# Kernel optimization log

Measured on AMD Instinct MI355X. Metric: run time of the kernel, lower is better.

## Reference

```python
import jax, jax.numpy as jnp
import numpy as np

NUM_HEADS = 4
D_MODEL = 256
HEAD_DIM = D_MODEL // NUM_HEADS  # 64
B, N = 8, 2048


def _proj(x, W, b):
    # Conv1d with kernel_size=1 == pointwise linear over channel dim
    # x: [B, C_in, N], W: [C_out, C_in], b: [C_out]
    return jnp.einsum('oi,bin->bon', W, x) + b[None, :, None]


def setup_inputs() -> dict:
    key = jax.random.key(0)
    ks = jax.random.split(key, 11)
    s = 1.0 / np.sqrt(D_MODEL)
    return {
        'query': jax.random.normal(ks[0], (B, D_MODEL, N), jnp.float32),
        'key':   jax.random.normal(ks[1], (B, D_MODEL, N), jnp.float32),
        'value': jax.random.normal(ks[2], (B, D_MODEL, N), jnp.float32),
        'Wq': jax.random.normal(ks[3], (D_MODEL, D_MODEL), jnp.float32) * s,
        'bq': jax.random.normal(ks[4], (D_MODEL,), jnp.float32) * 0.01,
        'Wk': jax.random.normal(ks[5], (D_MODEL, D_MODEL), jnp.float32) * s,
        'bk': jax.random.normal(ks[6], (D_MODEL,), jnp.float32) * 0.01,
        'Wv': jax.random.normal(ks[7], (D_MODEL, D_MODEL), jnp.float32) * s,
        'bv': jax.random.normal(ks[8], (D_MODEL,), jnp.float32) * 0.01,
        'Wm': jax.random.normal(ks[9], (D_MODEL, D_MODEL), jnp.float32) * s,
        'bm': jax.random.normal(ks[10], (D_MODEL,), jnp.float32) * 0.01,
    }


def reference(query, key, value, Wq, bq, Wk, bk, Wv, bv, Wm, bm):
    b = query.shape[0]
    # project then split channels into (head_dim, num_heads): [B, d, h, N]
    q = _proj(query, Wq, bq).reshape(b, HEAD_DIM, NUM_HEADS, -1)
    k = _proj(key,   Wk, bk).reshape(b, HEAD_DIM, NUM_HEADS, -1)
    v = _proj(value, Wv, bv).reshape(b, HEAD_DIM, NUM_HEADS, -1)
    scale = 1.0 / jnp.sqrt(jnp.asarray(HEAD_DIM, q.dtype))
    scores = jnp.einsum('bdhn,bdhm->bhnm', q, k) * scale  # [B,H,N,N]
    prob = jax.nn.softmax(scores, axis=-1)
    x = jnp.einsum('bhnm,bdhm->bdhn', prob, v)  # [B,d,H,N]
    x = x.reshape(b, HEAD_DIM * NUM_HEADS, -1)  # [B, d_model, N]
    return _proj(x, Wm, bm)
```

## Files before the change

### kernel.cpp

```cpp
#include <hip/hip_runtime.h>
#include <math.h>


constexpr int BATCH  = 8;
constexpr int DMODEL = 256;
constexpr int SEQ    = 2048;
constexpr int HDIM   = 64;
constexpr int TN     = 128;
constexpr int TM     = 64;
constexpr int NJT    = SEQ / TM;

typedef _Float16 half4_t __attribute__((ext_vector_type(4)));
typedef _Float16 half8_t __attribute__((ext_vector_type(8)));
typedef float    float4_t __attribute__((ext_vector_type(4)));

static __device__ __forceinline__ void ld16_lds(const void* g, void* l) {
    __builtin_amdgcn_global_load_lds(
        (const __attribute__((address_space(1))) unsigned*)g,
        (__attribute__((address_space(3))) unsigned*)l, 16, 0, 0);
}

__global__ __launch_bounds__(256)
void prep_w(const float* __restrict__ Wq, const float* __restrict__ Wk,
            const float* __restrict__ Wv, const float* __restrict__ Wm,
            _Float16* __restrict__ wf)
{
    const int which = blockIdx.y;
    const float* src = which == 0 ? Wq : which == 1 ? Wk : which == 2 ? Wv : Wm;
    const int i = (blockIdx.x * 256 + threadIdx.x) * 4;
    const float4 v = *(const float4*)&src[i];
    half4_t o; o[0] = v.x; o[1] = v.y; o[2] = v.z; o[3] = v.w;
    *(half4_t*)&wf[(size_t)which * DMODEL * DMODEL + i] = o;
}

__global__ __launch_bounds__(256, 3)
void gemm_qkv(const _Float16* __restrict__ wf, const float* __restrict__ bq,
              const float* __restrict__ bk, const float* __restrict__ bv,
              const float* __restrict__ Xq, const float* __restrict__ Xk,
              const float* __restrict__ Xv, _Float16* __restrict__ qT,
              _Float16* __restrict__ kT, _Float16* __restrict__ vT)
{
    const int n0 = blockIdx.x * 64;
    const int proj = blockIdx.y >> 3, b = blockIdx.y & 7;
    const _Float16* W    = wf + (size_t)proj * DMODEL * DMODEL;
    const float*    bias = proj == 0 ? bq : proj == 1 ? bk : bv;
    const float*    X    = (proj == 0 ? Xq : proj == 1 ? Xk : Xv)
                           + (size_t)b * DMODEL * SEQ;

    __shared__ __align__(16) char lds[50432];
    float*    T  = (float*)lds;
    _Float16* Xs = (_Float16*)(lds + 16640);
    _Float16* Tw = (_Float16*)lds;

    const int tid = threadIdx.x, tn = tid & 15, tc = tid >> 4;

    #pragma unroll
    for (int cc = 0; cc < 4; ++cc) {
        __syncthreads();
        #pragma unroll
        for (int i = 0; i < 4; ++i) {
            const int c = tc + 16 * i;
            const float4 v = *(const float4*)&X[(size_t)(cc * 64 + c) * SEQ + n0 + tn * 4];
            T[c * 65 + tn * 4 + 0] = v.x; T[c * 65 + tn * 4 + 1] = v.y;
            T[c * 65 + tn * 4 + 2] = v.z; T[c * 65 + tn * 4 + 3] = v.w;
        }
        __syncthreads();
        #pragma unroll
        for (int i = 0; i < 4; ++i) {
            const int n = tc + 16 * i;
            half4_t h4;
            #pragma unroll
            for (int j = 0; j < 4; ++j) h4[j] = (_Float16)T[(tn * 4 + j) * 65 + n];
            *(half4_t*)&Xs[n * 264 + cc * 64 + tn * 4] = h4;
        }
    }
    __syncthreads();

    const int w = tid >> 6, lane = tid & 63;
    const int lm = lane & 15, g = lane >> 4, g8 = g * 8;
    const int cw0 = w * 64;

    float4_t acc[4][4];
    #pragma unroll
    for (int mt = 0; mt < 4; ++mt)
        #pragma unroll
        for (int nt = 0; nt < 4; ++nt) acc[mt][nt] = (float4_t){0.f, 0.f, 0.f, 0.f};

    #pragma unroll
    for (int k0 = 0; k0 < DMODEL; k0 += 64) {
        half8_t a[4][2], bb[4][2];
        #pragma unroll
        for (int mt = 0; mt < 4; ++mt)
            #pragma unroll
            for (int kd = 0; kd < 2; ++kd)
                a[mt][kd] = *(const half8_t*)&W[(size_t)(cw0 + mt * 16 + lm) * DMODEL
                                                + k0 + kd * 32 + g8];
        #pragma unroll
        for (int nt = 0; nt < 4; ++nt)
            #pragma unroll
            for (int kd = 0; kd < 2; ++kd)
                bb[nt][kd] = *(const half8_t*)&Xs[(nt * 16 + lm) * 264
                                                  + k0 + kd * 32 + g8];
        #pragma unroll
        for (int kd = 0; kd < 2; ++kd)
            #pragma unroll
            for (int mt = 0; mt < 4; ++mt)
                #pragma unroll
                for (int nt = 0; nt < 4; ++nt)
                    acc[mt][nt] = __builtin_amdgcn_mfma_f32_16x16x32_f16(
                        a[mt][kd], bb[nt][kd], acc[mt][nt], 0, 0, 0);
    }
    __syncthreads();

    #pragma unroll
    for (int mt = 0; mt < 4; ++mt) {
        const float4 b4 = *(const float4*)&bias[cw0 + mt * 16 + g * 4];
        const float bb4[4] = {b4.x, b4.y, b4.z, b4.w};
        #pragma unroll
        for (int nt = 0; nt < 4; ++nt) {
            half4_t pk;
            #pragma unroll
            for (int r = 0; r < 4; ++r) pk[r] = (_Float16)(acc[mt][nt][r] + bb4[r]);
            *(half4_t*)&Tw[((w * 64 + nt * 16 + lm)) * 68 + mt * 16 + g * 4] = pk;
        }
    }

    if (proj < 2) {
        _Float16* dst = (proj == 0 ? qT : kT);
        const int h2 = lane >> 4, lml = lane & 15;
        #pragma unroll
        for (int it = 0; it < 4; ++it) {
            const int nl = it * 16 + lml;
            #pragma unroll
            for (int dc = 0; dc < 2; ++dc) {
                half8_t ch;
                #pragma unroll
                for (int e = 0; e < 8; ++e)
                    ch[e] = Tw[(w * 64 + nl) * 68 + 4 * (dc * 8 + e) + h2];
                const int chunk = (w * 2 + dc) ^ (nl & 7);
                *(half8_t*)&dst[((size_t)(b * 4 + h2) * SEQ + n0 + nl) * HDIM
                                + chunk * 8] = ch;
            }
        }
    } else {
        const int hh = lane & 3, dl = (lane >> 2) & 15;
        const int d = w * 16 + dl;
        const size_t rowbase =
            (((size_t)(b * 4 + hh) * NJT + (n0 >> 6)) * HDIM + d) * (size_t)TM;
        #pragma unroll
        for (int jc = 0; jc < 8; ++jc) {
            half8_t ch;
            #pragma unroll
            for (int e = 0; e < 8; ++e)
                ch[e] = Tw[(w * 64 + jc * 8 + e) * 68 + 4 * dl + hh];
            *(half8_t*)&vT[rowbase + ((jc ^ (dl & 7)) << 3)] = ch;
        }
    }
}

__global__ __launch_bounds__(256, 4)
void attn_f16(const _Float16* __restrict__ qT, const _Float16* __restrict__ kT,
              const _Float16* __restrict__ vT, _Float16* __restrict__ xa,
              _Float16* __restrict__ xb, float* __restrict__ rs)
{
    const int bh = blockIdx.z, b = bh >> 2, h = bh & 3;
    const int jh = blockIdx.y;
    const int tid = threadIdx.x, wid = tid >> 6, lane = tid & 63;
    const int lm = lane & 15, g = lane >> 4;
    const int i0 = blockIdx.x * TN + wid * 32;

    __shared__ _Float16 Kb[2][TM * HDIM];
    __shared__ _Float16 Vb[2][TM * HDIM];

    half8_t bq[2][2];
    const _Float16* qbase = qT + (size_t)bh * SEQ * HDIM;
    #pragma unroll
    for (int rt = 0; rt < 2; ++rt)
        #pragma unroll
        for (int kd = 0; kd < 2; ++kd) {
            const int row = i0 + rt * 16 + lm;
            half8_t r8 = *(const half8_t*)(qbase + (size_t)row * HDIM
                                           + (((kd * 4 + g) ^ (lm & 7)) << 3));
            #pragma unroll
            for (int e = 0; e < 8; ++e) r8[e] = r8[e] * (_Float16)0.125f;
            bq[rt][kd] = r8;
        }

    const char* kt = (const char*)(kT + ((size_t)bh * SEQ + jh * (SEQ / 2)) * HDIM);
    const char* vt = (const char*)(vT + ((size_t)bh * NJT + jh * 16) * TM * HDIM);

    float4_t o[2][4], o5[2];
    #pragma unroll
    for (int rt = 0; rt < 2; ++rt) {
        #pragma unroll
        for (int dt = 0; dt < 4; ++dt) o[rt][dt] = (float4_t){0.f, 0.f, 0.f, 0.f};
        o5[rt] = (float4_t){0.f, 0.f, 0.f, 0.f};
    }
    const half4_t vone = {(_Float16)1.f, (_Float16)1.f, (_Float16)1.f, (_Float16)1.f};

    #define STAGE(jt, bu)                                                     \
        {                                                                     \
            const char* kg = kt + (size_t)(jt) * 8192;                        \
            const char* vg = vt + (size_t)(jt) * 8192;                        \
            _Pragma("unroll")                                                 \
            for (int p = 0; p < 2; ++p) {                                     \
                const int c = wid + p * 4;                                    \
                ld16_lds(kg + c * 1024 + lane * 16, (char*)&Kb[bu][0] + c * 1024); \
                ld16_lds(vg + c * 1024 + lane * 16, (char*)&Vb[bu][0] + c * 1024); \
            }                                                                 \
        }

    STAGE(0, 0);
    __syncthreads();

    for (int jt = 0; jt < 16; ++jt) {
        const int cur = jt & 1;
        if (jt + 1 < 16) STAGE(jt + 1, cur ^ 1);

        float4_t s[4][2];
        #pragma unroll
        for (int ct = 0; ct < 4; ++ct)
            #pragma unroll
            for (int rt = 0; rt < 2; ++rt) s[ct][rt] = (float4_t){0.f, 0.f, 0.f, 0.f};
        #pragma unroll
        for (int kd = 0; kd < 2; ++kd)
            #pragma unroll
            for (int ct = 0; ct < 4; ++ct) {
                const half8_t fk = *(const half8_t*)
                    &Kb[cur][(ct * 16 + lm) * HDIM + (((kd * 4 + g) ^ (lm & 7)) << 3)];
                #pragma unroll
                for (int rt = 0; rt < 2; ++rt)
                    s[ct][rt] = __builtin_amdgcn_mfma_f32_16x16x32_f16(
                        fk, bq[rt][kd], s[ct][rt], 0, 0, 0);
            }

        half4_t ap[4][2];
        #pragma unroll
        for (int ct = 0; ct < 4; ++ct)
            #pragma unroll
            for (int rt = 0; rt < 2; ++rt)
                #pragma unroll
                for (int r = 0; r < 4; ++r)
                    ap[ct][rt][r] = (_Float16)__expf(s[ct][rt][r]);
        #pragma unroll
        for (int ct = 0; ct < 4; ++ct)
            #pragma unroll
            for (int rt = 0; rt < 2; ++rt)
                o5[rt] = __builtin_amdgcn_mfma_f32_16x16x16f16(
                    ap[ct][rt], vone, o5[rt], 0, 0, 0);

        #pragma unroll
        for (int ct = 0; ct < 4; ++ct)
            #pragma unroll
            for (int dt = 0; dt < 4; ++dt) {
                const int d = dt * 16 + lm;
                const half4_t fv = *(const half4_t*)
                    &Vb[cur][d * TM + ((((ct * 2 + (g >> 1)) ^ (lm & 7)) << 3)
                                       + ((g & 1) << 2))];
                #pragma unroll
                for (int rt = 0; rt < 2; ++rt)
                    o[rt][dt] = __builtin_amdgcn_mfma_f32_16x16x16f16(
                        ap[ct][rt], fv, o[rt][dt], 0, 0, 0);
            }
        __syncthreads();
    }

    _Float16* xp = jh ? xb : xa;
    #pragma unroll
    for (int rt = 0; rt < 2; ++rt)
        #pragma unroll
        for (int dt = 0; dt < 4; ++dt) {
            const int c = 4 * (dt * 16 + lm) + h;
            #pragma unroll
            for (int r = 0; r < 4; ++r) {
                const int n = i0 + rt * 16 + 4 * g + r;
                xp[((size_t)b * SEQ + n) * DMODEL + c] = (_Float16)o[rt][dt][r];
            }
        }
    if (lm == 0) {
        #pragma unroll
        for (int rt = 0; rt < 2; ++rt)
            #pragma unroll
            for (int r = 0; r < 4; ++r)
                rs[((size_t)jh * 32 + bh) * SEQ + i0 + rt * 16 + 4 * g + r] =
                    o5[rt][r];
    }
    #undef STAGE
}

__global__ __launch_bounds__(256)
void gemm_final(const _Float16* __restrict__ wm, const float* __restrict__ bias,
                const _Float16* __restrict__ xa, const _Float16* __restrict__ xb,
                const float* __restrict__ rs, float* __restrict__ out)
{
    const int n0 = blockIdx.x * 64, m0 = blockIdx.y * 128;
    const int b = blockIdx.z;
    const int tid = threadIdx.x, w = tid >> 6, lane = tid & 63;
    const int lm = lane & 15, g = lane >> 4, g8 = g * 8;
    const int cw0 = m0 + w * 32;

    const _Float16* Xa = xa + ((size_t)b * SEQ + n0) * DMODEL;
    const _Float16* Xb2 = xb + ((size_t)b * SEQ + n0) * DMODEL;

    half8_t pm[4];
    #pragma unroll
    for (int nt = 0; nt < 4; ++nt) {
        const int n = n0 + nt * 16 + lm;
        #pragma unroll
        for (int hh = 0; hh < 4; ++hh) {
            const float l = rs[(size_t)(b * 4 + hh) * SEQ + n]
                          + rs[(size_t)(32 + b * 4 + hh) * SEQ + n];
            const _Float16 iv = (_Float16)(1.0f / l);
            pm[nt][hh] = iv; pm[nt][hh + 4] = iv;
        }
    }

    float4_t acc[2][4];
    #pragma unroll
    for (int mt = 0; mt < 2; ++mt)
        #pragma unroll
        for (int nt = 0; nt < 4; ++nt) acc[mt][nt] = (float4_t){0.f, 0.f, 0.f, 0.f};

    #pragma unroll
    for (int k0 = 0; k0 < DMODEL; k0 += 64) {
        half8_t a[2][2], bb[4][2];
        #pragma unroll
        for (int mt = 0; mt < 2; ++mt)
            #pragma unroll
            for (int kd = 0; kd < 2; ++kd)
                a[mt][kd] = *(const half8_t*)&wm[(size_t)(cw0 + mt * 16 + lm) * DMODEL
                                                 + k0 + kd * 32 + g8];
        #pragma unroll
        for (int nt = 0; nt < 4; ++nt)
            #pragma unroll
            for (int kd = 0; kd < 2; ++kd) {
                const size_t off = (size_t)(nt * 16 + lm) * DMODEL + k0 + kd * 32 + g8;
                const half8_t va = *(const half8_t*)&Xa[off];
                const half8_t vb = *(const half8_t*)&Xb2[off];
                bb[nt][kd] = (va + vb) * pm[nt];
            }
        #pragma unroll
        for (int kd = 0; kd < 2; ++kd)
            #pragma unroll
            for (int mt = 0; mt < 2; ++mt)
                #pragma unroll
                for (int nt = 0; nt < 4; ++nt)
                    acc[mt][nt] = __builtin_amdgcn_mfma_f32_16x16x32_f16(
                        a[mt][kd], bb[nt][kd], acc[mt][nt], 0, 0, 0);
    }

    #pragma unroll
    for (int mt = 0; mt < 2; ++mt)
        #pragma unroll
        for (int r = 0; r < 4; ++r) {
            const int co = cw0 + mt * 16 + g * 4 + r;
            const float bv_ = bias[co];
            #pragma unroll
            for (int nt = 0; nt < 4; ++nt)
                out[((size_t)b * DMODEL + co) * SEQ + n0 + nt * 16 + lm] =
                    acc[mt][nt][r] + bv_;
        }
}

extern "C" void kernel_launch(void* const* d_in, const int* in_sizes, int n_in,
                              void* d_out, int out_size, void* d_ws, size_t ws_size,
                              hipStream_t stream) {
    const float* query = (const float*)d_in[0];
    const float* key_  = (const float*)d_in[1];
    const float* value = (const float*)d_in[2];
    const float* Wq = (const float*)d_in[3];  const float* bq = (const float*)d_in[4];
    const float* Wk = (const float*)d_in[5];  const float* bk = (const float*)d_in[6];
    const float* Wv = (const float*)d_in[7];  const float* bv = (const float*)d_in[8];
    const float* Wm = (const float*)d_in[9];  const float* bm = (const float*)d_in[10];
    float* out = (float*)d_out;

    const size_t bufElems = (size_t)BATCH * DMODEL * SEQ;
    _Float16* qT = (_Float16*)d_ws;
    _Float16* kT = qT + bufElems;
    _Float16* vT = kT + bufElems;
    _Float16* xa = vT + bufElems;
    _Float16* xb = xa + bufElems;
    _Float16* wf = xb + bufElems;
    float*    rsb = (float*)(wf + 4 * DMODEL * DMODEL);

    prep_w<<<dim3(DMODEL * DMODEL / 1024, 4), 256, 0, stream>>>(Wq, Wk, Wv, Wm, wf);
    gemm_qkv<<<dim3(SEQ / 64, 3 * BATCH), 256, 0, stream>>>(
        wf, bq, bk, bv, query, key_, value, qT, kT, vT);
    attn_f16<<<dim3(SEQ / TN, 2, BATCH * 4), 256, 0, stream>>>(qT, kT, vT, xa, xb, rsb);
    gemm_final<<<dim3(SEQ / 64, 2, BATCH), 256, 0, stream>>>(
        wf + (size_t)3 * DMODEL * DMODEL, bm, xa, xb, rsb, out);
}
```

Baseline: 195.4 us.

## Drop weight prep kernel, split attention keys four ways, restructure projection GEMMs

Removes the separate fp32-to-fp16 weight conversion kernel by converting weights inline in both GEMMs. The QKV GEMM now loads X straight from global memory with strided per-channel reads into a swizzled fp16 LDS tile, replacing the fp32 transpose staging. Attention splits the key range four ways instead of two, with the grid growing to match and the occupancy hint raised to 5, and writes four partial outputs plus interleaved row sums. The final GEMM reduces the four partials with smaller per-block output tiles. The aim is fewer launches and more parallel blocks, at the cost of extra partial-output traffic and redundant weight conversion per block.

```diff
diff --git a/kernel.cpp b/kernel.cpp
--- a/kernel.cpp
+++ b/kernel.cpp
@@ -10,6 +10,7 @@
 constexpr int TM     = 64;
 constexpr int NJT    = SEQ / TM;
 
+typedef _Float16 half2_t __attribute__((ext_vector_type(2)));
 typedef _Float16 half4_t __attribute__((ext_vector_type(4)));
 typedef _Float16 half8_t __attribute__((ext_vector_type(8)));
 typedef float    float4_t __attribute__((ext_vector_type(4)));
@@ -20,21 +21,16 @@
         (__attribute__((address_space(3))) unsigned*)l, 16, 0, 0);
 }
 
-__global__ __launch_bounds__(256)
-void prep_w(const float* __restrict__ Wq, const float* __restrict__ Wk,
-            const float* __restrict__ Wv, const float* __restrict__ Wm,
-            _Float16* __restrict__ wf)
-{
-    const int which = blockIdx.y;
-    const float* src = which == 0 ? Wq : which == 1 ? Wk : which == 2 ? Wv : Wm;
-    const int i = (blockIdx.x * 256 + threadIdx.x) * 4;
-    const float4 v = *(const float4*)&src[i];
-    half4_t o; o[0] = v.x; o[1] = v.y; o[2] = v.z; o[3] = v.w;
-    *(half4_t*)&wf[(size_t)which * DMODEL * DMODEL + i] = o;
-}
-
-__global__ __launch_bounds__(256, 3)
-void gemm_qkv(const _Float16* __restrict__ wf, const float* __restrict__ bq,
+static __device__ __forceinline__ half8_t pack8f(float4 x, float4 y) {
+    half8_t r;
+    r[0] = (_Float16)x.x; r[1] = (_Float16)x.y; r[2] = (_Float16)x.z; r[3] = (_Float16)x.w;
+    r[4] = (_Float16)y.x; r[5] = (_Float16)y.y; r[6] = (_Float16)y.z; r[7] = (_Float16)y.w;
+    return r;
+}
+
+__global__ __launch_bounds__(256, 4)
+void gemm_qkv(const float* __restrict__ Wq, const float* __restrict__ Wk,
+              const float* __restrict__ Wv, const float* __restrict__ bq,
               const float* __restrict__ bk, const float* __restrict__ bv,
               const float* __restrict__ Xq, const float* __restrict__ Xk,
               const float* __restrict__ Xv, _Float16* __restrict__ qT,
@@ -42,43 +38,35 @@
 {
     const int n0 = blockIdx.x * 64;
     const int proj = blockIdx.y >> 3, b = blockIdx.y & 7;
-    const _Float16* W    = wf + (size_t)proj * DMODEL * DMODEL;
-    const float*    bias = proj == 0 ? bq : proj == 1 ? bk : bv;
-    const float*    X    = (proj == 0 ? Xq : proj == 1 ? Xk : Xv)
-                           + (size_t)b * DMODEL * SEQ;
-
-    __shared__ __align__(16) char lds[50432];
-    float*    T  = (float*)lds;
-    _Float16* Xs = (_Float16*)(lds + 16640);
+    const float* W    = proj == 0 ? Wq : proj == 1 ? Wk : Wv;
+    const float* bias = proj == 0 ? bq : proj == 1 ? bk : bv;
+    const float* X    = (proj == 0 ? Xq : proj == 1 ? Xk : Xv)
+                        + (size_t)b * DMODEL * SEQ;
+
+    __shared__ __align__(16) char lds[36864];
+    _Float16* Xs = (_Float16*)lds;
     _Float16* Tw = (_Float16*)lds;
 
-    const int tid = threadIdx.x, tn = tid & 15, tc = tid >> 4;
-
-    #pragma unroll
-    for (int cc = 0; cc < 4; ++cc) {
-        __syncthreads();
-        #pragma unroll
-        for (int i = 0; i < 4; ++i) {
-            const int c = tc + 16 * i;
-            const float4 v = *(const float4*)&X[(size_t)(cc * 64 + c) * SEQ + n0 + tn * 4];
-            T[c * 65 + tn * 4 + 0] = v.x; T[c * 65 + tn * 4 + 1] = v.y;
-            T[c * 65 + tn * 4 + 2] = v.z; T[c * 65 + tn * 4 + 3] = v.w;
-        }
-        __syncthreads();
-        #pragma unroll
-        for (int i = 0; i < 4; ++i) {
-            const int n = tc + 16 * i;
-            half4_t h4;
-            #pragma unroll
-            for (int j = 0; j < 4; ++j) h4[j] = (_Float16)T[(tn * 4 + j) * 65 + n];
-            *(half4_t*)&Xs[n * 264 + cc * 64 + tn * 4] = h4;
+    const int tid = threadIdx.x, lane = tid & 63, wid = tid >> 6;
+
+    {
+        const float* Xn = X + n0 + lane;
+        _Float16* xrow = Xs + lane * 256;
+        const int nx = lane & 7;
+        #pragma unroll
+        for (int it = 0; it < 8; ++it) {
+            const int c8 = wid * 8 + it;
+            half8_t h;
+            #pragma unroll
+            for (int e = 0; e < 8; ++e)
+                h[e] = (_Float16)Xn[(size_t)(c8 * 8 + e) * SEQ];
+            *(half8_t*)&xrow[((c8 ^ nx) & 31) << 3] = h;
         }
     }
     __syncthreads();
 
-    const int w = tid >> 6, lane = tid & 63;
     const int lm = lane & 15, g = lane >> 4, g8 = g * 8;
-    const int cw0 = w * 64;
+    const int cw0 = wid * 64;
 
     float4_t acc[4][4];
     #pragma unroll
@@ -88,27 +76,26 @@
 
     #pragma unroll
     for (int k0 = 0; k0 < DMODEL; k0 += 64) {
-        half8_t a[4][2], bb[4][2];
-        #pragma unroll
-        for (int mt = 0; mt < 4; ++mt)
-            #pragma unroll
-            for (int kd = 0; kd < 2; ++kd)
-                a[mt][kd] = *(const half8_t*)&W[(size_t)(cw0 + mt * 16 + lm) * DMODEL
-                                                + k0 + kd * 32 + g8];
-        #pragma unroll
-        for (int nt = 0; nt < 4; ++nt)
-            #pragma unroll
-            for (int kd = 0; kd < 2; ++kd)
-                bb[nt][kd] = *(const half8_t*)&Xs[(nt * 16 + lm) * 264
-                                                  + k0 + kd * 32 + g8];
-        #pragma unroll
-        for (int kd = 0; kd < 2; ++kd)
+        #pragma unroll
+        for (int kd = 0; kd < 2; ++kd) {
+            half8_t a[4], bb[4];
+            #pragma unroll
+            for (int mt = 0; mt < 4; ++mt) {
+                const float* wp = W + (size_t)(cw0 + mt * 16 + lm) * DMODEL
+                                  + k0 + kd * 32 + g8;
+                a[mt] = pack8f(*(const float4*)wp, *(const float4*)(wp + 4));
+            }
+            #pragma unroll
+            for (int nt = 0; nt < 4; ++nt)
+                bb[nt] = *(const half8_t*)&Xs[(nt * 16 + lm) * 256 + k0
+                                              + (((kd * 4 + g) ^ (lm & 7)) << 3)];
             #pragma unroll
             for (int mt = 0; mt < 4; ++mt)
                 #pragma unroll
                 for (int nt = 0; nt < 4; ++nt)
                     acc[mt][nt] = __builtin_amdgcn_mfma_f32_16x16x32_f16(
-                        a[mt][kd], bb[nt][kd], acc[mt][nt], 0, 0, 0);
+                        a[mt], bb[nt], acc[mt][nt], 0, 0, 0);
+        }
     }
     __syncthreads();
 
@@ -121,7 +108,7 @@
             half4_t pk;
             #pragma unroll
             for (int r = 0; r < 4; ++r) pk[r] = (_Float16)(acc[mt][nt][r] + bb4[r]);
-            *(half4_t*)&Tw[((w * 64 + nt * 16 + lm)) * 68 + mt * 16 + g * 4] = pk;
+            *(half4_t*)&Tw[((size_t)(wid * 64 + nt * 16 + lm)) * 72 + mt * 16 + g * 4] = pk;
         }
     }
 
@@ -136,15 +123,15 @@
                 half8_t ch;
                 #pragma unroll
                 for (int e = 0; e < 8; ++e)
-                    ch[e] = Tw[(w * 64 + nl) * 68 + 4 * (dc * 8 + e) + h2];
-                const int chunk = (w * 2 + dc) ^ (nl & 7);
+                    ch[e] = Tw[(wid * 64 + nl) * 72 + 4 * (dc * 8 + e) + h2];
+                const int chunk = (wid * 2 + dc) ^ (nl & 7);
                 *(half8_t*)&dst[((size_t)(b * 4 + h2) * SEQ + n0 + nl) * HDIM
                                 + chunk * 8] = ch;
             }
         }
     } else {
         const int hh = lane & 3, dl = (lane >> 2) & 15;
-        const int d = w * 16 + dl;
+        const int d = wid * 16 + dl;
         const size_t rowbase =
             (((size_t)(b * 4 + hh) * NJT + (n0 >> 6)) * HDIM + d) * (size_t)TM;
         #pragma unroll
@@ -152,16 +139,16 @@
             half8_t ch;
             #pragma unroll
             for (int e = 0; e < 8; ++e)
-                ch[e] = Tw[(w * 64 + jc * 8 + e) * 68 + 4 * dl + hh];
+                ch[e] = Tw[(wid * 64 + jc * 8 + e) * 72 + 4 * dl + hh];
             *(half8_t*)&vT[rowbase + ((jc ^ (dl & 7)) << 3)] = ch;
         }
     }
 }
 
-__global__ __launch_bounds__(256, 4)
+__global__ __launch_bounds__(256, 5)
 void attn_f16(const _Float16* __restrict__ qT, const _Float16* __restrict__ kT,
-              const _Float16* __restrict__ vT, _Float16* __restrict__ xa,
-              _Float16* __restrict__ xb, float* __restrict__ rs)
+              const _Float16* __restrict__ vT, _Float16* __restrict__ xparts,
+              float* __restrict__ rs4)
 {
     const int bh = blockIdx.z, b = bh >> 2, h = bh & 3;
     const int jh = blockIdx.y;
@@ -186,8 +173,8 @@
             bq[rt][kd] = r8;
         }
 
-    const char* kt = (const char*)(kT + ((size_t)bh * SEQ + jh * (SEQ / 2)) * HDIM);
-    const char* vt = (const char*)(vT + ((size_t)bh * NJT + jh * 16) * TM * HDIM);
+    const char* kt = (const char*)(kT + ((size_t)bh * SEQ + jh * (SEQ / 4)) * HDIM);
+    const char* vt = (const char*)(vT + ((size_t)bh * NJT + jh * 8) * TM * HDIM);
 
     float4_t o[2][4], o5[2];
     #pragma unroll
@@ -213,9 +200,9 @@
     STAGE(0, 0);
     __syncthreads();
 
-    for (int jt = 0; jt < 16; ++jt) {
+    for (int jt = 0; jt < 8; ++jt) {
         const int cur = jt & 1;
-        if (jt + 1 < 16) STAGE(jt + 1, cur ^ 1);
+        if (jt + 1 < 8) STAGE(jt + 1, cur ^ 1);
 
         float4_t s[4][2];
         #pragma unroll
@@ -265,7 +252,7 @@
         __syncthreads();
     }
 
-    _Float16* xp = jh ? xb : xa;
+    _Float16* xp = xparts + (size_t)jh * BATCH * SEQ * DMODEL;
     #pragma unroll
     for (int rt = 0; rt < 2; ++rt)
         #pragma unroll
@@ -281,26 +268,27 @@
         #pragma unroll
         for (int rt = 0; rt < 2; ++rt)
             #pragma unroll
-            for (int r = 0; r < 4; ++r)
-                rs[((size_t)jh * 32 + bh) * SEQ + i0 + rt * 16 + 4 * g + r] =
-                    o5[rt][r];
+            for (int r = 0; r < 4; ++r) {
+                const int n = i0 + rt * 16 + 4 * g + r;
+                rs4[((size_t)bh * SEQ + n) * 4 + jh] = o5[rt][r];
+            }
     }
     #undef STAGE
 }
 
-__global__ __launch_bounds__(256)
-void gemm_final(const _Float16* __restrict__ wm, const float* __restrict__ bias,
-                const _Float16* __restrict__ xa, const _Float16* __restrict__ xb,
-                const float* __restrict__ rs, float* __restrict__ out)
+__global__ __launch_bounds__(256, 4)
+void gemm_final(const float* __restrict__ Wm, const float* __restrict__ bias,
+                const _Float16* __restrict__ xparts, const float* __restrict__ rs4,
+                float* __restrict__ out)
 {
-    const int n0 = blockIdx.x * 64, m0 = blockIdx.y * 128;
+    const int n0 = blockIdx.x * 64, co0 = blockIdx.y * 64;
     const int b = blockIdx.z;
     const int tid = threadIdx.x, w = tid >> 6, lane = tid & 63;
     const int lm = lane & 15, g = lane >> 4, g8 = g * 8;
-    const int cw0 = m0 + w * 32;
-
-    const _Float16* Xa = xa + ((size_t)b * SEQ + n0) * DMODEL;
-    const _Float16* Xb2 = xb + ((size_t)b * SEQ + n0) * DMODEL;
+    const int cw0 = co0 + w * 16;
+    const size_t PART = (size_t)BATCH * SEQ * DMODEL;
+
+    const _Float16* X0 = xparts + ((size_t)b * SEQ + n0) * DMODEL;
 
     half8_t pm[4];
     #pragma unroll
@@ -308,58 +296,44 @@
         const int n = n0 + nt * 16 + lm;
         #pragma unroll
         for (int hh = 0; hh < 4; ++hh) {
-            const float l = rs[(size_t)(b * 4 + hh) * SEQ + n]
-                          + rs[(size_t)(32 + b * 4 + hh) * SEQ + n];
-            const _Float16 iv = (_Float16)(1.0f / l);
+            const float4 r = *(const float4*)&rs4[((size_t)(b * 4 + hh) * SEQ + n) * 4];
+            const _Float16 iv = (_Float16)(1.0f / (r.x + r.y + r.z + r.w));
             pm[nt][hh] = iv; pm[nt][hh + 4] = iv;
         }
     }
 
-    float4_t acc[2][4];
-    #pragma unroll
-    for (int mt = 0; mt < 2; ++mt)
-        #pragma unroll
-        for (int nt = 0; nt < 4; ++nt) acc[mt][nt] = (float4_t){0.f, 0.f, 0.f, 0.f};
+    float4_t acc[4];
+    #pragma unroll
+    for (int nt = 0; nt < 4; ++nt) acc[nt] = (float4_t){0.f, 0.f, 0.f, 0.f};
 
     #pragma unroll
     for (int k0 = 0; k0 < DMODEL; k0 += 64) {
-        half8_t a[2][2], bb[4][2];
-        #pragma unroll
-        for (int mt = 0; mt < 2; ++mt)
-            #pragma unroll
-            for (int kd = 0; kd < 2; ++kd)
-                a[mt][kd] = *(const half8_t*)&wm[(size_t)(cw0 + mt * 16 + lm) * DMODEL
-                                                 + k0 + kd * 32 + g8];
+        #pragma unroll
+        for (int kd = 0; kd < 2; ++kd) {
+            const float* wp = Wm + (size_t)(cw0 + lm) * DMODEL + k0 + kd * 32 + g8;
+            const half8_t a = pack8f(*(const float4*)wp, *(const float4*)(wp + 4));
+            #pragma unroll
+            for (int nt = 0; nt < 4; ++nt) {
+                const size_t off = (size_t)(nt * 16 + lm) * DMODEL + k0 + kd * 32 + g8;
+                const half8_t sum = *(const half8_t*)&X0[off]
+                                  + *(const half8_t*)&X0[off + PART]
+                                  + *(const half8_t*)&X0[off + 2 * PART]
+                                  + *(const half8_t*)&X0[off + 3 * PART];
+                acc[nt] = __builtin_amdgcn_mfma_f32_16x16x32_f16(
+                    a, sum * pm[nt], acc[nt], 0, 0, 0);
+            }
+        }
+    }
+
+    #pragma unroll
+    for (int r = 0; r < 4; ++r) {
+        const int co = cw0 + g * 4 + r;
+        const float bv_ = bias[co];
         #pragma unroll
         for (int nt = 0; nt < 4; ++nt)
-            #pragma unroll
-            for (int kd = 0; kd < 2; ++kd) {
-                const size_t off = (size_t)(nt * 16 + lm) * DMODEL + k0 + kd * 32 + g8;
-                const half8_t va = *(const half8_t*)&Xa[off];
-                const half8_t vb = *(const half8_t*)&Xb2[off];
-                bb[nt][kd] = (va + vb) * pm[nt];
-            }
-        #pragma unroll
-        for (int kd = 0; kd < 2; ++kd)
-            #pragma unroll
-            for (int mt = 0; mt < 2; ++mt)
-                #pragma unroll
-                for (int nt = 0; nt < 4; ++nt)
-                    acc[mt][nt] = __builtin_amdgcn_mfma_f32_16x16x32_f16(
-                        a[mt][kd], bb[nt][kd], acc[mt][nt], 0, 0, 0);
-    }
-
-    #pragma unroll
-    for (int mt = 0; mt < 2; ++mt)
-        #pragma unroll
-        for (int r = 0; r < 4; ++r) {
-            const int co = cw0 + mt * 16 + g * 4 + r;
-            const float bv_ = bias[co];
-            #pragma unroll
-            for (int nt = 0; nt < 4; ++nt)
-                out[((size_t)b * DMODEL + co) * SEQ + n0 + nt * 16 + lm] =
-                    acc[mt][nt][r] + bv_;
-        }
+            out[((size_t)b * DMODEL + co) * SEQ + n0 + nt * 16 + lm] =
+                acc[nt][r] + bv_;
+    }
 }
 
 extern "C" void kernel_launch(void* const* d_in, const int* in_sizes, int n_in,
@@ -378,15 +352,13 @@
     _Float16* qT = (_Float16*)d_ws;
     _Float16* kT = qT + bufElems;
     _Float16* vT = kT + bufElems;
-    _Float16* xa = vT + bufElems;
-    _Float16* xb = xa + bufElems;
-    _Float16* wf = xb + bufElems;
-    float*    rsb = (float*)(wf + 4 * DMODEL * DMODEL);
-
-    prep_w<<<dim3(DMODEL * DMODEL / 1024, 4), 256, 0, stream>>>(Wq, Wk, Wv, Wm, wf);
+    _Float16* xparts = vT + bufElems;
+    float*    rs4 = (float*)(xparts + 4 * bufElems);
+
     gemm_qkv<<<dim3(SEQ / 64, 3 * BATCH), 256, 0, stream>>>(
-        wf, bq, bk, bv, query, key_, value, qT, kT, vT);
-    attn_f16<<<dim3(SEQ / TN, 2, BATCH * 4), 256, 0, stream>>>(qT, kT, vT, xa, xb, rsb);
-    gemm_final<<<dim3(SEQ / 64, 2, BATCH), 256, 0, stream>>>(
-        wf + (size_t)3 * DMODEL * DMODEL, bm, xa, xb, rsb, out);
-}
+        Wq, Wk, Wv, bq, bk, bv, query, key_, value, qT, kT, vT);
+    attn_f16<<<dim3(SEQ / TN, 4, BATCH * 4), 256, 0, stream>>>(
+        qT, kT, vT, xparts, rs4);
+    gemm_final<<<dim3(SEQ / 64, 4, BATCH), 256, 0, stream>>>(
+        Wm, bm, xparts, rs4, out);
+}
```

Measured after the change: 343.5 us. +75.8%, slower.
